# Kernel optimization log

Hardware: AMD Instinct MI355X
Metric: run time of the kernel (lower is better)

The kernel has to match this reference:

```python
import jax, jax.numpy as jnp
import numpy as np

C = 256          # channels
H = 8            # attn_heads
B = 2048         # number of graphs
NPG = 128        # nodes per graph
N = B * NPG      # total nodes
EPS = 1e-5


def setup_inputs() -> dict:
    key = jax.random.key(0)
    ks = jax.random.split(key, 16)
    s = 1.0 / np.sqrt(C)
    seg = jnp.repeat(jnp.arange(B, dtype=jnp.int32), NPG)          # sorted, all segments present
    batch = jnp.stack([seg, seg], axis=1)                           # [N, 2]; column 0 = graph id
    return {
        "x": jax.random.normal(ks[0], (N, C), dtype=jnp.float32),
        "batch": batch,
        "num_graphs": B,
        "W1": jax.random.normal(ks[1], (C, C), dtype=jnp.float32) * s,
        "b1": jnp.zeros((C,), jnp.float32),
        "gamma": jnp.ones((C,), jnp.float32),
        "beta": jnp.zeros((C,), jnp.float32),
        "W2": jax.random.normal(ks[2], (C, C), dtype=jnp.float32) * s,
        "b2": jnp.zeros((C,), jnp.float32),
        "Wq": jax.random.normal(ks[3], (C, C), dtype=jnp.float32) * s,
        "bq": jnp.zeros((C,), jnp.float32),
        "Wk": jax.random.normal(ks[4], (C, C), dtype=jnp.float32) * s,
        "bk": jnp.zeros((C,), jnp.float32),
        "Wv": jax.random.normal(ks[5], (C, C), dtype=jnp.float32) * s,
        "bv": jnp.zeros((C,), jnp.float32),
        "Wo": jax.random.normal(ks[6], (C, C), dtype=jnp.float32) * s,
        "bo": jnp.zeros((C,), jnp.float32),
        "Wr": jax.random.normal(ks[7], (1, C), dtype=jnp.float32) * s,
        "br": jnp.zeros((1,), jnp.float32),
    }


def reference(x, batch, num_graphs, W1, b1, gamma, beta, W2, b2,
              Wq, bq, Wk, bk, Wv, bv, Wo, bo, Wr, br):
    seg = batch[:, 0]                                   # [N] graph ids, sorted
    Dh = C // H
    scale = 1.0 / np.sqrt(Dh)

    # trunk: Linear -> BatchNorm1d (train-mode batch stats) -> ReLU -> Linear
    h = x @ W1.T + b1                                   # [N, C]
    mu = h.mean(axis=0)
    var = h.var(axis=0)                                 # biased, as torch uses for normalization
    h = (h - mu) * jax.lax.rsqrt(var + EPS) * gamma + beta
    h = jax.nn.relu(h)
    h = h @ W2.T + b2                                   # [N, C]

    # single-query MHA pooled per graph segment (query = ones(C))
    q = jnp.ones((C,), h.dtype)
    qh = (q @ Wq.T + bq).reshape(H, Dh)                 # [H, Dh] shared across graphs
    kh = (h @ Wk.T + bk).reshape(N, H, Dh)              # [N, H, Dh]
    vh = (h @ Wv.T + bv).reshape(N, H, Dh)

    logits = jnp.einsum('nhd,hd->nh', kh, qh) * scale   # [N, H]
    # segment softmax over each graph's nodes
    m = jax.ops.segment_max(logits, seg, num_segments=num_graphs)   # [B, H]
    p = jnp.exp(logits - m[seg])                                     # [N, H]
    denom = jax.ops.segment_sum(p, seg, num_segments=num_graphs)     # [B, H]
    attn = p / denom[seg]                                            # [N, H]

    pooled = jax.ops.segment_sum(attn[:, :, None] * vh, seg,
                                 num_segments=num_graphs)            # [B, H, Dh]
    pooled = pooled.reshape(num_graphs, C) @ Wo.T + bo               # out_proj -> [B, C]

    out = jnp.tanh(pooled @ Wr.T + br)                               # [B, 1]
    return out
```

## Files before the change

### kernel.cpp

```cpp
#include <hip/hip_runtime.h>
#include <hip/hip_bf16.h>
#include <math.h>

#define C_DIM 256
#define H_HEADS 8
#define B_GRAPHS 2048
#define NPG 128
#define N_NODES (B_GRAPHS * NPG)
#define EPS 1e-5f
#define SCALE_ATT 0.17677669529663687f
#define AST 264

typedef short bf16x8 __attribute__((ext_vector_type(8)));
typedef float f32x4 __attribute__((ext_vector_type(4)));

__device__ __forceinline__ unsigned short f2bf(float f) {
    __hip_bfloat16 h = __float2bfloat16(f);
    union { __hip_bfloat16 h; unsigned short u; } cv; cv.h = h; return cv.u;
}
__device__ __forceinline__ float bf2f(unsigned short u) {
    union { unsigned int i; float f; } v; v.i = ((unsigned int)u) << 16; return v.f;
}


__global__ __launch_bounds__(256) void prep1_kernel(
    const float* __restrict__ Wq, const float* __restrict__ bq,
    const float* __restrict__ Wk,
    const float* __restrict__ Wo, const float* __restrict__ Wr,
    float* __restrict__ wk_eff, float* __restrict__ wor)
{
    __shared__ float qhS[256];
    __shared__ float WrS[256];
    const int t = threadIdx.x;
    {
        float s = bq[t];
        const float* row = Wq + (size_t)t * 256;
        for (int c = 0; c < 256; c += 4) {
            float4 v = *(const float4*)&row[c];
            s += v.x + v.y + v.z + v.w;
        }
        qhS[t] = s;
        WrS[t] = Wr[t];
    }
    __syncthreads();
    for (int it = 0; it < 8; ++it) {
        int idx = t + it * 256;
        int head = idx >> 8, c = idx & 255;
        float acc = 0.f;
        #pragma unroll 4
        for (int d = 0; d < 32; ++d)
            acc = fmaf(Wk[(size_t)(head * 32 + d) * 256 + c], qhS[head * 32 + d], acc);
        wk_eff[head * 256 + c] = acc * SCALE_ATT;
    }
    {
        float acc = 0.f;
        for (int j2 = 0; j2 < 256; ++j2)
            acc = fmaf(Wo[(size_t)j2 * 256 + t], WrS[j2], acc);
        wor[t] = acc;
    }
}

__global__ __launch_bounds__(256) void prep2_kernel(
    const float* __restrict__ W2, const float* __restrict__ Wv,
    const float* __restrict__ wk_eff, const float* __restrict__ wor_g,
    unsigned short* __restrict__ WBg, float* __restrict__ V_g)
{
    __shared__ float wkS[256];
    const int t = threadIdx.x, head = blockIdx.x;
    wkS[t] = wk_eff[head * 256 + t];
    __syncthreads();
    float acc = 0.f;
    #pragma unroll 4
    for (int cp = 0; cp < 256; ++cp)
        acc = fmaf(W2[(size_t)cp * 256 + t], wkS[cp], acc);
    WBg[head * 256 + t] = f2bf(acc);
    float accv = 0.f;
    #pragma unroll 4
    for (int d = 0; d < 32; ++d) {
        int j = head * 32 + d;
        accv = fmaf(Wv[(size_t)j * 256 + t], wor_g[j], accv);
    }
    V_g[head * 256 + t] = accv;
}

__global__ __launch_bounds__(256) void prep3_kernel(
    const float* __restrict__ W2, const float* __restrict__ V_g,
    unsigned short* __restrict__ WBg)
{
    __shared__ float vS[256];
    const int t = threadIdx.x, head = blockIdx.x;
    vS[t] = V_g[head * 256 + t];
    __syncthreads();
    float acc = 0.f;
    #pragma unroll 4
    for (int cp = 0; cp < 256; ++cp)
        acc = fmaf(W2[(size_t)cp * 256 + t], vS[cp], acc);
    WBg[(8 + head) * 256 + t] = f2bf(acc);
}

__global__ __launch_bounds__(256) void prep4_kernel(
    const float* __restrict__ b2, const float* __restrict__ bv,
    const float* __restrict__ bo, const float* __restrict__ Wr,
    const float* __restrict__ br, const float* __restrict__ V_g,
    const float* __restrict__ wor, float* __restrict__ c0)
{
    __shared__ float red[256];
    const int t = threadIdx.x;
    float vs = 0.f;
    #pragma unroll
    for (int h = 0; h < 8; ++h) vs += V_g[h * 256 + t];
    red[t] = b2[t] * vs + bv[t] * wor[t] + bo[t] * Wr[t];
    __syncthreads();
    for (int s = 128; s > 0; s >>= 1) {
        if (t < s) red[t] += red[t + s];
        __syncthreads();
    }
    if (t == 0) c0[0] = red[0] + br[0];
}

__global__ __launch_bounds__(256) void w1cvt_kernel(
    const float* __restrict__ W1, unsigned short* __restrict__ W1bf)
{
    int i = blockIdx.x * 256 + threadIdx.x;
    W1bf[i] = f2bf(W1[i]);
}

__global__ __launch_bounds__(256) void gemm1_kernel(
    const float* __restrict__ x, const unsigned short* __restrict__ W1bf,
    unsigned short* __restrict__ h1s,
    float* __restrict__ parts1, float* __restrict__ parts2)
{
    __shared__ unsigned short Alds[128 * 40];
    __shared__ unsigned short Blds[256 * 40];
    const int t = threadIdx.x;
    const int lane = t & 63, w = t >> 6;
    const int l15 = lane & 15, kg = lane >> 4;
    const size_t n0 = (size_t)blockIdx.x * 128;

    f32x4 acc[2][16];
    #pragma unroll
    for (int mt = 0; mt < 2; ++mt)
        #pragma unroll
        for (int nt = 0; nt < 16; ++nt)
            acc[mt][nt] = (f32x4){0.f, 0.f, 0.f, 0.f};

    for (int kk = 0; kk < 8; ++kk) {
        if (kk) __syncthreads();
        #pragma unroll
        for (int p = 0; p < 4; ++p) {
            int i = p * 256 + t;
            {
                int row = i >> 3, kq = i & 7;
                float4 v = *(const float4*)&x[(n0 + row) * 256 + kk * 32 + kq * 4];
                ushort4 u;
                u.x = f2bf(v.x); u.y = f2bf(v.y); u.z = f2bf(v.z); u.w = f2bf(v.w);
                *(ushort4*)&Alds[row * 40 + kq * 4] = u;
            }
            {
                int row = i >> 2, seg = i & 3;
                bf16x8 bv = *(const bf16x8*)&W1bf[(size_t)row * 256 + kk * 32 + seg * 8];
                *(bf16x8*)&Blds[row * 40 + seg * 8] = bv;
            }
        }
        __syncthreads();
        bf16x8 a0 = *(const bf16x8*)&Alds[(w * 32 + l15) * 40 + kg * 8];
        bf16x8 a1 = *(const bf16x8*)&Alds[(w * 32 + 16 + l15) * 40 + kg * 8];
        #pragma unroll
        for (int nt = 0; nt < 16; ++nt) {
            bf16x8 b = *(const bf16x8*)&Blds[(nt * 16 + l15) * 40 + kg * 8];
            acc[0][nt] = __builtin_amdgcn_mfma_f32_16x16x32_bf16(a0, b, acc[0][nt], 0, 0, 0);
            acc[1][nt] = __builtin_amdgcn_mfma_f32_16x16x32_bf16(a1, b, acc[1][nt], 0, 0, 0);
        }
    }

    float s1[16], s2[16];
    #pragma unroll
    for (int nt = 0; nt < 16; ++nt) { s1[nt] = 0.f; s2[nt] = 0.f; }
    const size_t rowqBase = (n0 >> 2) + (size_t)w * 8;
    #pragma unroll
    for (int mt = 0; mt < 2; ++mt)
        #pragma unroll
        for (int nt = 0; nt < 16; ++nt) {
            float f0 = acc[mt][nt][0], f1 = acc[mt][nt][1];
            float f2v = acc[mt][nt][2], f3 = acc[mt][nt][3];
            s1[nt] += (f0 + f1) + (f2v + f3);
            s2[nt] += (f0 * f0 + f1 * f1) + (f2v * f2v + f3 * f3);
            ushort4 u;
            u.x = f2bf(f0); u.y = f2bf(f1); u.z = f2bf(f2v); u.w = f2bf(f3);
            *(ushort4*)&h1s[(rowqBase + mt * 4 + kg) * 1024 + (nt * 16 + l15) * 4] = u;
        }
    #pragma unroll
    for (int nt = 0; nt < 16; ++nt) {
        s1[nt] += __shfl_xor(s1[nt], 16);
        s1[nt] += __shfl_xor(s1[nt], 32);
        s2[nt] += __shfl_xor(s2[nt], 16);
        s2[nt] += __shfl_xor(s2[nt], 32);
    }
    if (lane < 16) {
        size_t prow = ((size_t)blockIdx.x * 4 + w) * 256;
        #pragma unroll
        for (int nt = 0; nt < 16; ++nt) {
            parts1[prow + nt * 16 + lane] = s1[nt];
            parts2[prow + nt * 16 + lane] = s2[nt];
        }
    }
}

__global__ __launch_bounds__(256) void reduce_kernel(
    const float* __restrict__ P1, const float* __restrict__ P2,
    float* __restrict__ psum, float* __restrict__ psum2)
{
    const int t = threadIdx.x;
    const int b = blockIdx.x;
    float s = 0.f, s2 = 0.f;
    for (int r = 0; r < 128; ++r) {
        size_t row = (size_t)(b * 128 + r) * 256;
        s += P1[row + t];
        s2 += P2[row + t];
    }
    atomicAdd(&psum[t], s);
    atomicAdd(&psum2[t], s2);
}

__global__ __launch_bounds__(256) void stats_kernel(
    const float* __restrict__ psum, const float* __restrict__ psum2,
    const float* __restrict__ gamma, const float* __restrict__ beta,
    float* __restrict__ sc, float* __restrict__ sh)
{
    const int t = threadIdx.x;
    const float invN = 1.0f / (float)N_NODES;
    float S = psum[t], S2 = psum2[t];
    float mu = S * invN;
    float var = S2 * invN - mu * mu;
    float rstd = rsqrtf(var + EPS);
    float g = gamma[t] * rstd;
    sc[t] = g;
    sh[t] = beta[t] - mu * g;
}

__global__ __launch_bounds__(256, 1) void fused_kernel(
    const unsigned short* __restrict__ h1s, const float* __restrict__ sc_g,
    const float* __restrict__ sh_g, const unsigned short* __restrict__ WBg,
    const float* __restrict__ c0_g, float* __restrict__ out)
{
    __shared__ __align__(16) unsigned short aS[128 * AST];
    __shared__ __align__(16) unsigned short WBl[16 * AST];
    __shared__ float scS[256], shS[256];
    __shared__ float LG[128 * 17];
    __shared__ float redH[8];
    __shared__ float c0S;

    const int t = threadIdx.x;
    const int g = blockIdx.x;
    const int lane = t & 63, w = t >> 6;
    const int l15 = lane & 15, kg = lane >> 4;

    scS[t] = sc_g[t];
    shS[t] = sh_g[t];
    {
        int j = t >> 4, cc = (t & 15) * 16;
        bf16x8 w0 = *(const bf16x8*)&WBg[j * 256 + cc];
        bf16x8 w1 = *(const bf16x8*)&WBg[j * 256 + cc + 8];
        *(bf16x8*)&WBl[j * AST + cc] = w0;
        *(bf16x8*)&WBl[j * AST + cc + 8] = w1;
    }
    if (t == 0) c0S = c0_g[0];
    __syncthreads();

    const unsigned short* hg = h1s + (size_t)g * 32768;
    unsigned int* aS32 = (unsigned int*)aS;
    #pragma unroll 4
    for (int it = 0; it < 16; ++it) {
        int i = it * 256 + t;
        int rowq = i >> 7, cp = i & 127, cc0 = cp * 2;
        bf16x8 hv = *(const bf16x8*)&hg[rowq * 1024 + cp * 8];
        float sc0 = scS[cc0], sc1 = scS[cc0 + 1];
        float sh0 = shS[cc0], sh1 = shS[cc0 + 1];
        #pragma unroll
        for (int r = 0; r < 4; ++r) {
            float a0 = fmaxf(fmaf(bf2f((unsigned short)hv[r]), sc0, sh0), 0.f);
            float a1 = fmaxf(fmaf(bf2f((unsigned short)hv[r + 4]), sc1, sh1), 0.f);
            unsigned int pk = (unsigned int)f2bf(a0) | ((unsigned int)f2bf(a1) << 16);
            aS32[((rowq * 4 + r) * AST + cc0) >> 1] = pk;
        }
    }
    __syncthreads();

    {
        const int m0 = w * 32;
        f32x4 acc0 = {0.f, 0.f, 0.f, 0.f}, acc1 = {0.f, 0.f, 0.f, 0.f};
        #pragma unroll
        for (int kt = 0; kt < 8; ++kt) {
            bf16x8 b  = *(const bf16x8*)&WBl[l15 * AST + kt * 32 + kg * 8];
            bf16x8 a0 = *(const bf16x8*)&aS[(m0 + l15) * AST + kt * 32 + kg * 8];
            bf16x8 a1 = *(const bf16x8*)&aS[(m0 + 16 + l15) * AST + kt * 32 + kg * 8];
            acc0 = __builtin_amdgcn_mfma_f32_16x16x32_bf16(a0, b, acc0, 0, 0, 0);
            acc1 = __builtin_amdgcn_mfma_f32_16x16x32_bf16(a1, b, acc1, 0, 0, 0);
        }
        #pragma unroll
        for (int r = 0; r < 4; ++r) {
            LG[(m0 + kg * 4 + r) * 17 + l15] = acc0[r];
            LG[(m0 + 16 + kg * 4 + r) * 17 + l15] = acc1[r];
        }
    }
    __syncthreads();

    {
        const int h = t >> 5, j = t & 31;
        float l[4], gv[4];
        #pragma unroll
        for (int q = 0; q < 4; ++q) {
            int n = j + q * 32;
            l[q]  = LG[n * 17 + h];
            gv[q] = LG[n * 17 + 8 + h];
        }
        float m = fmaxf(fmaxf(l[0], l[1]), fmaxf(l[2], l[3]));
        for (int s = 16; s > 0; s >>= 1) m = fmaxf(m, __shfl_xor(m, s, 32));
        float sp = 0.f, sg = 0.f;
        #pragma unroll
        for (int q = 0; q < 4; ++q) {
            float p = expf(l[q] - m);
            sp += p;
            sg = fmaf(p, gv[q], sg);
        }
        for (int s = 16; s > 0; s >>= 1) {
            sp += __shfl_xor(sp, s, 32);
            sg += __shfl_xor(sg, s, 32);
        }
        if (j == 0) redH[h] = sg / sp;
    }
    __syncthreads();
    if (t == 0) {
        float r = c0S;
        #pragma unroll
        for (int h = 0; h < 8; ++h) r += redH[h];
        out[g] = tanhf(r);
    }
}

#define FOFF_WKE 0
#define FOFF_WOR 2048
#define FOFF_V   2304
#define FOFF_C0  4352
#define FOFF_PS  4368
#define FOFF_PS2 4624
#define FOFF_SC  4880
#define FOFF_SH  5136
#define FOFF_P1  5392
#define FOFF_P2  (5392 + 2097152)

extern "C" void kernel_launch(void* const* d_in, const int* in_sizes, int n_in,
                              void* d_out, int out_size, void* d_ws, size_t ws_size,
                              hipStream_t stream)
{
    (void)in_sizes; (void)n_in; (void)out_size; (void)ws_size;
    const float* x     = (const float*)d_in[0];
    const float* W1    = (const float*)d_in[3];
    const float* gamma = (const float*)d_in[5];
    const float* beta  = (const float*)d_in[6];
    const float* W2    = (const float*)d_in[7];
    const float* b2    = (const float*)d_in[8];
    const float* Wq    = (const float*)d_in[9];
    const float* bq    = (const float*)d_in[10];
    const float* Wk    = (const float*)d_in[11];
    const float* Wv    = (const float*)d_in[13];
    const float* bv    = (const float*)d_in[14];
    const float* Wo    = (const float*)d_in[15];
    const float* bo    = (const float*)d_in[16];
    const float* Wr    = (const float*)d_in[17];
    const float* br    = (const float*)d_in[18];

    unsigned short* h1s  = (unsigned short*)d_ws;
    unsigned short* W1bf = h1s + (size_t)N_NODES * 256;
    unsigned short* WBg  = W1bf + 65536;
    float* fbase = (float*)(WBg + 4096);

    float* wk_eff = fbase + FOFF_WKE;
    float* wor    = fbase + FOFF_WOR;
    float* V_g    = fbase + FOFF_V;
    float* c0     = fbase + FOFF_C0;
    float* psum   = fbase + FOFF_PS;
    float* psum2  = fbase + FOFF_PS2;
    float* sc     = fbase + FOFF_SC;
    float* sh     = fbase + FOFF_SH;
    float* P1     = fbase + FOFF_P1;
    float* P2     = fbase + FOFF_P2;

    hipMemsetAsync((void*)psum, 0, 512 * sizeof(float), stream);

    hipLaunchKernelGGL(prep1_kernel, dim3(1), dim3(256), 0, stream,
                       Wq, bq, Wk, Wo, Wr, wk_eff, wor);
    hipLaunchKernelGGL(w1cvt_kernel, dim3(256), dim3(256), 0, stream, W1, W1bf);
    hipLaunchKernelGGL(prep2_kernel, dim3(8), dim3(256), 0, stream,
                       W2, Wv, wk_eff, wor, WBg, V_g);
    hipLaunchKernelGGL(prep3_kernel, dim3(8), dim3(256), 0, stream, W2, V_g, WBg);
    hipLaunchKernelGGL(prep4_kernel, dim3(1), dim3(256), 0, stream,
                       b2, bv, bo, Wr, br, V_g, wor, c0);
    hipLaunchKernelGGL(gemm1_kernel, dim3(N_NODES / 128), dim3(256), 0, stream,
                       x, W1bf, h1s, P1, P2);
    hipLaunchKernelGGL(reduce_kernel, dim3(64), dim3(256), 0, stream, P1, P2, psum, psum2);
    hipLaunchKernelGGL(stats_kernel, dim3(1), dim3(256), 0, stream,
                       psum, psum2, gamma, beta, sc, sh);
    hipLaunchKernelGGL(fused_kernel, dim3(B_GRAPHS), dim3(256), 0, stream,
                       h1s, sc, sh, WBg, c0, (float*)d_out);
}
```

Measured before the change: 586.8 us.

## Collapse prep, stats and reduce kernels into three launches with row-major h1

Merges the W1 conversion and the first prep step into one launch, and folds the W2/Wv projection prep into extra blocks of the main GEMM. BN statistics are now reduced inside the GEMM through LDS and global atomics, which removes the partial-sum buffers and the separate reduce and stats kernels. The intermediate h1 is stored row-major, and the pooling kernel reads it straight from global memory into MFMA operands without staging the whole tile in LDS. This cuts launch count and intermediate traffic, at the cost of heavier atomic contention and a different global access pattern in the final kernel.

```diff
diff --git a/kernel.cpp b/kernel.cpp
--- a/kernel.cpp
+++ b/kernel.cpp
@@ -9,7 +9,6 @@
 #define N_NODES (B_GRAPHS * NPG)
 #define EPS 1e-5f
 #define SCALE_ATT 0.17677669529663687f
-#define AST 264
 
 typedef short bf16x8 __attribute__((ext_vector_type(8)));
 typedef float f32x4 __attribute__((ext_vector_type(4)));
@@ -22,16 +21,21 @@
     union { unsigned int i; float f; } v; v.i = ((unsigned int)u) << 16; return v.f;
 }
 
-
-__global__ __launch_bounds__(256) void prep1_kernel(
+__global__ __launch_bounds__(256) void prepA_kernel(
+    const float* __restrict__ W1, unsigned short* __restrict__ W1bf,
     const float* __restrict__ Wq, const float* __restrict__ bq,
-    const float* __restrict__ Wk,
-    const float* __restrict__ Wo, const float* __restrict__ Wr,
+    const float* __restrict__ Wk, const float* __restrict__ Wo,
+    const float* __restrict__ Wr,
     float* __restrict__ wk_eff, float* __restrict__ wor)
 {
     __shared__ float qhS[256];
     __shared__ float WrS[256];
     const int t = threadIdx.x;
+    if (blockIdx.x < 256) {
+        int i = blockIdx.x * 256 + t;
+        W1bf[i] = f2bf(W1[i]);
+        return;
+    }
     {
         float s = bq[t];
         const float* row = Wq + (size_t)t * 256;
@@ -43,14 +47,12 @@
         WrS[t] = Wr[t];
     }
     __syncthreads();
-    for (int it = 0; it < 8; ++it) {
-        int idx = t + it * 256;
-        int head = idx >> 8, c = idx & 255;
+    for (int head = 0; head < 8; ++head) {
         float acc = 0.f;
         #pragma unroll 4
         for (int d = 0; d < 32; ++d)
-            acc = fmaf(Wk[(size_t)(head * 32 + d) * 256 + c], qhS[head * 32 + d], acc);
-        wk_eff[head * 256 + c] = acc * SCALE_ATT;
+            acc = fmaf(Wk[(size_t)(head * 32 + d) * 256 + t], qhS[head * 32 + d], acc);
+        wk_eff[head * 256 + t] = acc * SCALE_ATT;
     }
     {
         float acc = 0.f;
@@ -60,89 +62,70 @@
     }
 }
 
-__global__ __launch_bounds__(256) void prep2_kernel(
+__global__ __launch_bounds__(256) void gemm_kernel(
+    const float* __restrict__ x, const unsigned short* __restrict__ W1bf,
+    unsigned short* __restrict__ h1,
+    float* __restrict__ psum, float* __restrict__ psum2,
     const float* __restrict__ W2, const float* __restrict__ Wv,
-    const float* __restrict__ wk_eff, const float* __restrict__ wor_g,
-    unsigned short* __restrict__ WBg, float* __restrict__ V_g)
-{
-    __shared__ float wkS[256];
-    const int t = threadIdx.x, head = blockIdx.x;
-    wkS[t] = wk_eff[head * 256 + t];
-    __syncthreads();
-    float acc = 0.f;
-    #pragma unroll 4
-    for (int cp = 0; cp < 256; ++cp)
-        acc = fmaf(W2[(size_t)cp * 256 + t], wkS[cp], acc);
-    WBg[head * 256 + t] = f2bf(acc);
-    float accv = 0.f;
-    #pragma unroll 4
-    for (int d = 0; d < 32; ++d) {
-        int j = head * 32 + d;
-        accv = fmaf(Wv[(size_t)j * 256 + t], wor_g[j], accv);
-    }
-    V_g[head * 256 + t] = accv;
-}
-
-__global__ __launch_bounds__(256) void prep3_kernel(
-    const float* __restrict__ W2, const float* __restrict__ V_g,
-    unsigned short* __restrict__ WBg)
-{
-    __shared__ float vS[256];
-    const int t = threadIdx.x, head = blockIdx.x;
-    vS[t] = V_g[head * 256 + t];
-    __syncthreads();
-    float acc = 0.f;
-    #pragma unroll 4
-    for (int cp = 0; cp < 256; ++cp)
-        acc = fmaf(W2[(size_t)cp * 256 + t], vS[cp], acc);
-    WBg[(8 + head) * 256 + t] = f2bf(acc);
-}
-
-__global__ __launch_bounds__(256) void prep4_kernel(
+    const float* __restrict__ wk_eff, const float* __restrict__ wor,
     const float* __restrict__ b2, const float* __restrict__ bv,
     const float* __restrict__ bo, const float* __restrict__ Wr,
-    const float* __restrict__ br, const float* __restrict__ V_g,
-    const float* __restrict__ wor, float* __restrict__ c0)
+    const float* __restrict__ br,
+    unsigned short* __restrict__ WBg, float* __restrict__ c0)
 {
-    __shared__ float red[256];
+    __shared__ unsigned short Wlds[256 * 40];
+    __shared__ unsigned short Xlds[128 * 40];
+    __shared__ float red1[256], red2[256];
+    __shared__ float worS[32];
     const int t = threadIdx.x;
-    float vs = 0.f;
-    #pragma unroll
-    for (int h = 0; h < 8; ++h) vs += V_g[h * 256 + t];
-    red[t] = b2[t] * vs + bv[t] * wor[t] + bo[t] * Wr[t];
-    __syncthreads();
-    for (int s = 128; s > 0; s >>= 1) {
-        if (t < s) red[t] += red[t + s];
+
+    if (blockIdx.x >= 2048) {
+        const int head = blockIdx.x - 2048;
+        float* wkS = red1;
+        float* vS  = red2;
+        wkS[t] = wk_eff[head * 256 + t];
+        if (t < 32) worS[t] = wor[head * 32 + t];
         __syncthreads();
-    }
-    if (t == 0) c0[0] = red[0] + br[0];
-}
-
-__global__ __launch_bounds__(256) void w1cvt_kernel(
-    const float* __restrict__ W1, unsigned short* __restrict__ W1bf)
-{
-    int i = blockIdx.x * 256 + threadIdx.x;
-    W1bf[i] = f2bf(W1[i]);
-}
-
-__global__ __launch_bounds__(256) void gemm1_kernel(
-    const float* __restrict__ x, const unsigned short* __restrict__ W1bf,
-    unsigned short* __restrict__ h1s,
-    float* __restrict__ parts1, float* __restrict__ parts2)
-{
-    __shared__ unsigned short Alds[128 * 40];
-    __shared__ unsigned short Blds[256 * 40];
-    const int t = threadIdx.x;
+        float acc = 0.f;
+        #pragma unroll 4
+        for (int cp = 0; cp < 256; ++cp)
+            acc = fmaf(W2[(size_t)cp * 256 + t], wkS[cp], acc);
+        WBg[head * 256 + t] = f2bf(acc);
+        float accv = 0.f;
+        #pragma unroll 4
+        for (int d = 0; d < 32; ++d)
+            accv = fmaf(Wv[(size_t)(head * 32 + d) * 256 + t], worS[d], accv);
+        vS[t] = accv;
+        __syncthreads();
+        float accg = 0.f;
+        #pragma unroll 4
+        for (int cp = 0; cp < 256; ++cp)
+            accg = fmaf(W2[(size_t)cp * 256 + t], vS[cp], accg);
+        WBg[(8 + head) * 256 + t] = f2bf(accg);
+        float part = b2[t] * accv;
+        if (head == 0) {
+            part += bv[t] * wor[t] + bo[t] * Wr[t];
+            if (t == 0) part += br[0];
+        }
+        #pragma unroll
+        for (int s = 1; s < 64; s <<= 1) part += __shfl_xor(part, s);
+        if ((t & 63) == 0) atomicAdd(c0, part);
+        return;
+    }
+
     const int lane = t & 63, w = t >> 6;
     const int l15 = lane & 15, kg = lane >> 4;
     const size_t n0 = (size_t)blockIdx.x * 128;
 
-    f32x4 acc[2][16];
-    #pragma unroll
-    for (int mt = 0; mt < 2; ++mt)
-        #pragma unroll
-        for (int nt = 0; nt < 16; ++nt)
-            acc[mt][nt] = (f32x4){0.f, 0.f, 0.f, 0.f};
+    red1[t] = 0.f;
+    red2[t] = 0.f;
+
+    f32x4 acc0[16], acc1[16];
+    #pragma unroll
+    for (int mt = 0; mt < 16; ++mt) {
+        acc0[mt] = (f32x4){0.f, 0.f, 0.f, 0.f};
+        acc1[mt] = (f32x4){0.f, 0.f, 0.f, 0.f};
+    }
 
     for (int kk = 0; kk < 8; ++kk) {
         if (kk) __syncthreads();
@@ -154,154 +137,121 @@
                 float4 v = *(const float4*)&x[(n0 + row) * 256 + kk * 32 + kq * 4];
                 ushort4 u;
                 u.x = f2bf(v.x); u.y = f2bf(v.y); u.z = f2bf(v.z); u.w = f2bf(v.w);
-                *(ushort4*)&Alds[row * 40 + kq * 4] = u;
+                *(ushort4*)&Xlds[row * 40 + kq * 4] = u;
             }
             {
                 int row = i >> 2, seg = i & 3;
-                bf16x8 bv = *(const bf16x8*)&W1bf[(size_t)row * 256 + kk * 32 + seg * 8];
-                *(bf16x8*)&Blds[row * 40 + seg * 8] = bv;
+                bf16x8 bv8 = *(const bf16x8*)&W1bf[(size_t)row * 256 + kk * 32 + seg * 8];
+                *(bf16x8*)&Wlds[row * 40 + seg * 8] = bv8;
             }
         }
         __syncthreads();
-        bf16x8 a0 = *(const bf16x8*)&Alds[(w * 32 + l15) * 40 + kg * 8];
-        bf16x8 a1 = *(const bf16x8*)&Alds[(w * 32 + 16 + l15) * 40 + kg * 8];
-        #pragma unroll
-        for (int nt = 0; nt < 16; ++nt) {
-            bf16x8 b = *(const bf16x8*)&Blds[(nt * 16 + l15) * 40 + kg * 8];
-            acc[0][nt] = __builtin_amdgcn_mfma_f32_16x16x32_bf16(a0, b, acc[0][nt], 0, 0, 0);
-            acc[1][nt] = __builtin_amdgcn_mfma_f32_16x16x32_bf16(a1, b, acc[1][nt], 0, 0, 0);
-        }
-    }
-
-    float s1[16], s2[16];
-    #pragma unroll
-    for (int nt = 0; nt < 16; ++nt) { s1[nt] = 0.f; s2[nt] = 0.f; }
-    const size_t rowqBase = (n0 >> 2) + (size_t)w * 8;
-    #pragma unroll
-    for (int mt = 0; mt < 2; ++mt)
-        #pragma unroll
-        for (int nt = 0; nt < 16; ++nt) {
-            float f0 = acc[mt][nt][0], f1 = acc[mt][nt][1];
-            float f2v = acc[mt][nt][2], f3 = acc[mt][nt][3];
-            s1[nt] += (f0 + f1) + (f2v + f3);
-            s2[nt] += (f0 * f0 + f1 * f1) + (f2v * f2v + f3 * f3);
-            ushort4 u;
-            u.x = f2bf(f0); u.y = f2bf(f1); u.z = f2bf(f2v); u.w = f2bf(f3);
-            *(ushort4*)&h1s[(rowqBase + mt * 4 + kg) * 1024 + (nt * 16 + l15) * 4] = u;
-        }
-    #pragma unroll
-    for (int nt = 0; nt < 16; ++nt) {
-        s1[nt] += __shfl_xor(s1[nt], 16);
-        s1[nt] += __shfl_xor(s1[nt], 32);
-        s2[nt] += __shfl_xor(s2[nt], 16);
-        s2[nt] += __shfl_xor(s2[nt], 32);
-    }
-    if (lane < 16) {
-        size_t prow = ((size_t)blockIdx.x * 4 + w) * 256;
-        #pragma unroll
-        for (int nt = 0; nt < 16; ++nt) {
-            parts1[prow + nt * 16 + lane] = s1[nt];
-            parts2[prow + nt * 16 + lane] = s2[nt];
-        }
-    }
-}
-
-__global__ __launch_bounds__(256) void reduce_kernel(
-    const float* __restrict__ P1, const float* __restrict__ P2,
-    float* __restrict__ psum, float* __restrict__ psum2)
-{
-    const int t = threadIdx.x;
-    const int b = blockIdx.x;
-    float s = 0.f, s2 = 0.f;
-    for (int r = 0; r < 128; ++r) {
-        size_t row = (size_t)(b * 128 + r) * 256;
-        s += P1[row + t];
-        s2 += P2[row + t];
-    }
-    atomicAdd(&psum[t], s);
-    atomicAdd(&psum2[t], s2);
-}
-
-__global__ __launch_bounds__(256) void stats_kernel(
+        bf16x8 b0 = *(const bf16x8*)&Xlds[(w * 32 + l15) * 40 + kg * 8];
+        bf16x8 b1 = *(const bf16x8*)&Xlds[(w * 32 + 16 + l15) * 40 + kg * 8];
+        #pragma unroll
+        for (int mt = 0; mt < 16; ++mt) {
+            bf16x8 a = *(const bf16x8*)&Wlds[(mt * 16 + l15) * 40 + kg * 8];
+            acc0[mt] = __builtin_amdgcn_mfma_f32_16x16x32_bf16(a, b0, acc0[mt], 0, 0, 0);
+            acc1[mt] = __builtin_amdgcn_mfma_f32_16x16x32_bf16(a, b1, acc1[mt], 0, 0, 0);
+        }
+    }
+
+    const size_t rb0 = (n0 + w * 32 + l15) * 256;
+    const size_t rb1 = rb0 + 16 * 256;
+    #pragma unroll
+    for (int mt = 0; mt < 16; ++mt) {
+        f32x4 a0 = acc0[mt], a1 = acc1[mt];
+        ushort4 u0, u1;
+        u0.x = f2bf(a0[0]); u0.y = f2bf(a0[1]); u0.z = f2bf(a0[2]); u0.w = f2bf(a0[3]);
+        u1.x = f2bf(a1[0]); u1.y = f2bf(a1[1]); u1.z = f2bf(a1[2]); u1.w = f2bf(a1[3]);
+        *(ushort4*)&h1[rb0 + mt * 16 + kg * 4] = u0;
+        *(ushort4*)&h1[rb1 + mt * 16 + kg * 4] = u1;
+        float s1v[4], s2v[4];
+        #pragma unroll
+        for (int r = 0; r < 4; ++r) {
+            s1v[r] = a0[r] + a1[r];
+            s2v[r] = a0[r] * a0[r] + a1[r] * a1[r];
+        }
+        #pragma unroll
+        for (int r = 0; r < 4; ++r) {
+            #pragma unroll
+            for (int s = 1; s < 16; s <<= 1) {
+                s1v[r] += __shfl_xor(s1v[r], s);
+                s2v[r] += __shfl_xor(s2v[r], s);
+            }
+        }
+        if (l15 == 0) {
+            #pragma unroll
+            for (int r = 0; r < 4; ++r) {
+                atomicAdd(&red1[mt * 16 + kg * 4 + r], s1v[r]);
+                atomicAdd(&red2[mt * 16 + kg * 4 + r], s2v[r]);
+            }
+        }
+    }
+    __syncthreads();
+    atomicAdd(&psum[t], red1[t]);
+    atomicAdd(&psum2[t], red2[t]);
+}
+
+__global__ __launch_bounds__(256) void fused_kernel(
+    const unsigned short* __restrict__ h1,
     const float* __restrict__ psum, const float* __restrict__ psum2,
     const float* __restrict__ gamma, const float* __restrict__ beta,
-    float* __restrict__ sc, float* __restrict__ sh)
-{
-    const int t = threadIdx.x;
-    const float invN = 1.0f / (float)N_NODES;
-    float S = psum[t], S2 = psum2[t];
-    float mu = S * invN;
-    float var = S2 * invN - mu * mu;
-    float rstd = rsqrtf(var + EPS);
-    float g = gamma[t] * rstd;
-    sc[t] = g;
-    sh[t] = beta[t] - mu * g;
-}
-
-__global__ __launch_bounds__(256, 1) void fused_kernel(
-    const unsigned short* __restrict__ h1s, const float* __restrict__ sc_g,
-    const float* __restrict__ sh_g, const unsigned short* __restrict__ WBg,
+    const unsigned short* __restrict__ WBg,
     const float* __restrict__ c0_g, float* __restrict__ out)
 {
-    __shared__ __align__(16) unsigned short aS[128 * AST];
-    __shared__ __align__(16) unsigned short WBl[16 * AST];
     __shared__ float scS[256], shS[256];
     __shared__ float LG[128 * 17];
     __shared__ float redH[8];
-    __shared__ float c0S;
 
     const int t = threadIdx.x;
     const int g = blockIdx.x;
     const int lane = t & 63, w = t >> 6;
     const int l15 = lane & 15, kg = lane >> 4;
 
-    scS[t] = sc_g[t];
-    shS[t] = sh_g[t];
     {
-        int j = t >> 4, cc = (t & 15) * 16;
-        bf16x8 w0 = *(const bf16x8*)&WBg[j * 256 + cc];
-        bf16x8 w1 = *(const bf16x8*)&WBg[j * 256 + cc + 8];
-        *(bf16x8*)&WBl[j * AST + cc] = w0;
-        *(bf16x8*)&WBl[j * AST + cc + 8] = w1;
-    }
-    if (t == 0) c0S = c0_g[0];
-    __syncthreads();
-
-    const unsigned short* hg = h1s + (size_t)g * 32768;
-    unsigned int* aS32 = (unsigned int*)aS;
-    #pragma unroll 4
-    for (int it = 0; it < 16; ++it) {
-        int i = it * 256 + t;
-        int rowq = i >> 7, cp = i & 127, cc0 = cp * 2;
-        bf16x8 hv = *(const bf16x8*)&hg[rowq * 1024 + cp * 8];
-        float sc0 = scS[cc0], sc1 = scS[cc0 + 1];
-        float sh0 = shS[cc0], sh1 = shS[cc0 + 1];
-        #pragma unroll
-        for (int r = 0; r < 4; ++r) {
-            float a0 = fmaxf(fmaf(bf2f((unsigned short)hv[r]), sc0, sh0), 0.f);
-            float a1 = fmaxf(fmaf(bf2f((unsigned short)hv[r + 4]), sc1, sh1), 0.f);
-            unsigned int pk = (unsigned int)f2bf(a0) | ((unsigned int)f2bf(a1) << 16);
-            aS32[((rowq * 4 + r) * AST + cc0) >> 1] = pk;
-        }
-    }
-    __syncthreads();
-
-    {
-        const int m0 = w * 32;
-        f32x4 acc0 = {0.f, 0.f, 0.f, 0.f}, acc1 = {0.f, 0.f, 0.f, 0.f};
-        #pragma unroll
-        for (int kt = 0; kt < 8; ++kt) {
-            bf16x8 b  = *(const bf16x8*)&WBl[l15 * AST + kt * 32 + kg * 8];
-            bf16x8 a0 = *(const bf16x8*)&aS[(m0 + l15) * AST + kt * 32 + kg * 8];
-            bf16x8 a1 = *(const bf16x8*)&aS[(m0 + 16 + l15) * AST + kt * 32 + kg * 8];
-            acc0 = __builtin_amdgcn_mfma_f32_16x16x32_bf16(a0, b, acc0, 0, 0, 0);
-            acc1 = __builtin_amdgcn_mfma_f32_16x16x32_bf16(a1, b, acc1, 0, 0, 0);
-        }
-        #pragma unroll
-        for (int r = 0; r < 4; ++r) {
-            LG[(m0 + kg * 4 + r) * 17 + l15] = acc0[r];
-            LG[(m0 + 16 + kg * 4 + r) * 17 + l15] = acc1[r];
-        }
+        const float invN = 1.0f / (float)N_NODES;
+        float S = psum[t], S2 = psum2[t];
+        float mu = S * invN;
+        float var = S2 * invN - mu * mu;
+        float rstd = rsqrtf(var + EPS);
+        float gmr = gamma[t] * rstd;
+        scS[t] = gmr;
+        shS[t] = beta[t] - mu * gmr;
+    }
+    bf16x8 af[8];
+    #pragma unroll
+    for (int kt = 0; kt < 8; ++kt)
+        af[kt] = *(const bf16x8*)&WBg[l15 * 256 + kt * 32 + kg * 8];
+    __syncthreads();
+
+    const size_t base0 = ((size_t)g * 128 + w * 32 + l15) * 256;
+    const size_t base1 = base0 + 16 * 256;
+    f32x4 acc0 = {0.f, 0.f, 0.f, 0.f}, acc1 = {0.f, 0.f, 0.f, 0.f};
+    #pragma unroll
+    for (int kt = 0; kt < 8; ++kt) {
+        const int cc = kt * 32 + kg * 8;
+        bf16x8 h0 = *(const bf16x8*)&h1[base0 + cc];
+        bf16x8 h1v = *(const bf16x8*)&h1[base1 + cc];
+        f32x4 scA = *(const f32x4*)&scS[cc];
+        f32x4 scB = *(const f32x4*)&scS[cc + 4];
+        f32x4 shA = *(const f32x4*)&shS[cc];
+        f32x4 shB = *(const f32x4*)&shS[cc + 4];
+        bf16x8 b0, b1;
+        #pragma unroll
+        for (int e = 0; e < 4; ++e) {
+            b0[e]     = (short)f2bf(fmaxf(fmaf(bf2f((unsigned short)h0[e]),      scA[e], shA[e]), 0.f));
+            b0[e + 4] = (short)f2bf(fmaxf(fmaf(bf2f((unsigned short)h0[e + 4]),  scB[e], shB[e]), 0.f));
+            b1[e]     = (short)f2bf(fmaxf(fmaf(bf2f((unsigned short)h1v[e]),     scA[e], shA[e]), 0.f));
+            b1[e + 4] = (short)f2bf(fmaxf(fmaf(bf2f((unsigned short)h1v[e + 4]), scB[e], shB[e]), 0.f));
+        }
+        acc0 = __builtin_amdgcn_mfma_f32_16x16x32_bf16(af[kt], b0, acc0, 0, 0, 0);
+        acc1 = __builtin_amdgcn_mfma_f32_16x16x32_bf16(af[kt], b1, acc1, 0, 0, 0);
+    }
+    #pragma unroll
+    for (int r = 0; r < 4; ++r) {
+        LG[(w * 32 + l15) * 17 + kg * 4 + r]      = acc0[r];
+        LG[(w * 32 + 16 + l15) * 17 + kg * 4 + r] = acc1[r];
     }
     __syncthreads();
 
@@ -331,23 +281,12 @@
     }
     __syncthreads();
     if (t == 0) {
-        float r = c0S;
+        float r = c0_g[0];
         #pragma unroll
         for (int h = 0; h < 8; ++h) r += redH[h];
         out[g] = tanhf(r);
     }
 }
-
-#define FOFF_WKE 0
-#define FOFF_WOR 2048
-#define FOFF_V   2304
-#define FOFF_C0  4352
-#define FOFF_PS  4368
-#define FOFF_PS2 4624
-#define FOFF_SC  4880
-#define FOFF_SH  5136
-#define FOFF_P1  5392
-#define FOFF_P2  (5392 + 2097152)
 
 extern "C" void kernel_launch(void* const* d_in, const int* in_sizes, int n_in,
                               void* d_out, int out_size, void* d_ws, size_t ws_size,
@@ -370,37 +309,24 @@
     const float* Wr    = (const float*)d_in[17];
     const float* br    = (const float*)d_in[18];
 
-    unsigned short* h1s  = (unsigned short*)d_ws;
-    unsigned short* W1bf = h1s + (size_t)N_NODES * 256;
+    unsigned short* h1   = (unsigned short*)d_ws;
+    unsigned short* W1bf = h1 + (size_t)N_NODES * 256;
     unsigned short* WBg  = W1bf + 65536;
     float* fbase = (float*)(WBg + 4096);
 
-    float* wk_eff = fbase + FOFF_WKE;
-    float* wor    = fbase + FOFF_WOR;
-    float* V_g    = fbase + FOFF_V;
-    float* c0     = fbase + FOFF_C0;
-    float* psum   = fbase + FOFF_PS;
-    float* psum2  = fbase + FOFF_PS2;
-    float* sc     = fbase + FOFF_SC;
-    float* sh     = fbase + FOFF_SH;
-    float* P1     = fbase + FOFF_P1;
-    float* P2     = fbase + FOFF_P2;
-
-    hipMemsetAsync((void*)psum, 0, 512 * sizeof(float), stream);
-
-    hipLaunchKernelGGL(prep1_kernel, dim3(1), dim3(256), 0, stream,
-                       Wq, bq, Wk, Wo, Wr, wk_eff, wor);
-    hipLaunchKernelGGL(w1cvt_kernel, dim3(256), dim3(256), 0, stream, W1, W1bf);
-    hipLaunchKernelGGL(prep2_kernel, dim3(8), dim3(256), 0, stream,
-                       W2, Wv, wk_eff, wor, WBg, V_g);
-    hipLaunchKernelGGL(prep3_kernel, dim3(8), dim3(256), 0, stream, W2, V_g, WBg);
-    hipLaunchKernelGGL(prep4_kernel, dim3(1), dim3(256), 0, stream,
-                       b2, bv, bo, Wr, br, V_g, wor, c0);
-    hipLaunchKernelGGL(gemm1_kernel, dim3(N_NODES / 128), dim3(256), 0, stream,
-                       x, W1bf, h1s, P1, P2);
-    hipLaunchKernelGGL(reduce_kernel, dim3(64), dim3(256), 0, stream, P1, P2, psum, psum2);
-    hipLaunchKernelGGL(stats_kernel, dim3(1), dim3(256), 0, stream,
-                       psum, psum2, gamma, beta, sc, sh);
+    float* wk_eff = fbase;
+    float* wor    = fbase + 2048;
+    float* psum   = fbase + 2304;
+    float* psum2  = fbase + 2560;
+    float* c0     = fbase + 2816;
+
+    hipMemsetAsync((void*)psum, 0, 513 * sizeof(float), stream);
+
+    hipLaunchKernelGGL(prepA_kernel, dim3(257), dim3(256), 0, stream,
+                       W1, W1bf, Wq, bq, Wk, Wo, Wr, wk_eff, wor);
+    hipLaunchKernelGGL(gemm_kernel, dim3(2056), dim3(256), 0, stream,
+                       x, W1bf, h1, psum, psum2,
+                       W2, Wv, wk_eff, wor, b2, bv, bo, Wr, br, WBg, c0);
     hipLaunchKernelGGL(fused_kernel, dim3(B_GRAPHS), dim3(256), 0, stream,
-                       h1s, sc, sh, WBg, c0, (float*)d_out);
-}
+                       h1, psum, psum2, gamma, beta, WBg, c0, (float*)d_out);
+}
```

Result: no change. 597.9 us (+1.9%).
